# Kernel tuning notes

Hardware: AMD Instinct MI355X
Metric: run time of the kernel (lower is better)

## Reference

```python
import jax, jax.numpy as jnp
import numpy as np

RNN = 64

def linear(x, W, b):
    return x @ W.T + b

def sample_logprob(key, logits):
    # Categorical(softmax(logits)): sample + log_prob of the sample
    s = jax.random.categorical(key, logits)
    lp = jnp.take_along_axis(jax.nn.log_softmax(logits, -1), s[:, None], 1)[:, 0]
    return s, lp

def lstm_encode(inst, embed, W_ih, W_hh, b_ih, b_hh):
    # torch.nn.LSTMCell unrolled over the sequence; gate order i,f,g,o
    x = embed[inst]                              # [B,S,64]
    B = inst.shape[0]
    def step(carry, xt):
        h, c = carry
        gates = xt @ W_ih.T + b_ih + h @ W_hh.T + b_hh   # [B,256]
        i, f, g, o = jnp.split(gates, 4, axis=-1)
        c = jax.nn.sigmoid(f) * c + jax.nn.sigmoid(i) * jnp.tanh(g)
        h = jax.nn.sigmoid(o) * jnp.tanh(c)
        return (h, c), None
    h0 = jnp.zeros((B, RNN), x.dtype)
    (h, _), _ = jax.lax.scan(step, (h0, h0), jnp.swapaxes(x, 0, 1))
    return h

def setup_inputs():
    key = jax.random.key(0)
    ks = jax.random.split(key, 20)
    B, S, V = 16384, 32, 1000
    def nrm(k, shape, scale=0.05):
        return jax.random.normal(k, shape, jnp.float32) * scale
    return {
        "inst0": jax.random.randint(ks[0], (B, S), 0, V + 1),
        "inst1": jax.random.randint(ks[1], (B, S), 0, V + 1),
        "canvas0": jax.random.randint(ks[2], (B, 25, 4), 0, 5).astype(jnp.int32),
        "canvas1": jax.random.randint(ks[3], (B, 25, 4), 0, 5).astype(jnp.int32),
        "ref": jax.random.randint(ks[4], (B, 4), 0, 5).astype(jnp.int32),
        "embed": nrm(ks[5], (V + 1, RNN)),
        "W_ih": nrm(ks[6], (4 * RNN, RNN)), "W_hh": nrm(ks[7], (4 * RNN, RNN)),
        "b_ih": jnp.zeros(4 * RNN), "b_hh": jnp.zeros(4 * RNN),
        "Wc": nrm(ks[8], (3, RNN)), "bc": jnp.zeros(3),
        "Ws": nrm(ks[9], (3, RNN)), "bs": jnp.zeros(3),
        "Wl": nrm(ks[10], (25, RNN)), "bl": jnp.zeros(25),
        "Wr1": nrm(ks[11], (32, RNN + 4)), "br1": jnp.zeros(32),
        "Wr2": nrm(ks[12], (1, 32)), "br2": jnp.zeros(1),
        "Wp": nrm(ks[13], (8, RNN)), "bp": jnp.zeros(8),
    }

def reference(inst0, inst1, canvas0, canvas1, ref, embed, W_ih, W_hh, b_ih, b_hh,
              Wc, bc, Ws, bs, Wl, bl, Wr1, br1, Wr2, br2, Wp, bp):
    B = inst0.shape[0]
    kk = jax.random.split(jax.random.key(42), 7)
    final_canvas = canvas1                                   # [B,25,4]

    def step_rewards(loc_predict, color_sample, shape_sample):
        valid = (loc_predict >= 0) & (loc_predict < 25)
        pt = jnp.take_along_axis(final_canvas,
                                 jnp.clip(loc_predict, 0, 24)[:, None, None],
                                 axis=1)[:, 0]               # [B,4]
        ok = valid & (pt.sum(-1) >= 0)
        loc_r = jnp.where(ok, 1.0, -1.0)
        col_r = jnp.where(ok, jnp.where(color_sample == pt[:, 0], 1.0, -1.0), 0.0)
        shp_r = jnp.where(ok, jnp.where(shape_sample == pt[:, 1], 1.0, -1.0), 0.0)
        return loc_r, col_r, shp_r

    # ---- dialog step 0: absolute location ----
    h0 = lstm_encode(inst0, embed, W_ih, W_hh, b_ih, b_hh)
    cs0, clp0 = sample_logprob(kk[0], linear(h0, Wc, bc))
    ss0, slp0 = sample_logprob(kk[1], linear(h0, Ws, bs))
    loc0, llp0 = sample_logprob(kk[2], linear(h0, Wl, bl))
    loc_r0, col_r0, _ = step_rewards(loc0, cs0, ss0)

    # ---- dialog step 1: relative location w.r.t. attended ref object ----
    h1 = lstm_encode(inst1, embed, W_ih, W_hh, b_ih, b_hh)
    cs1, clp1 = sample_logprob(kk[3], linear(h1, Wc, bc))
    ss1, slp1 = sample_logprob(kk[4], linear(h1, Ws, bs))
    ls1, llp1 = sample_logprob(kk[5], linear(h1, Wp, bp))    # 8-way offset
    prev = canvas0.astype(h1.dtype)                          # [B,25,4]
    feat = jnp.concatenate([jnp.broadcast_to(h1[:, None, :], (B, 25, RNN)), prev], 2)  # [B,25,68]
    att_logits = (jax.nn.relu(feat @ Wr1.T + br1) @ Wr2.T + br2)[:, :, 0]              # [B,25]
    att_sample, alp1 = sample_logprob(kk[6], att_logits)
    ref_obj = jnp.take_along_axis(canvas0, att_sample[:, None, None], axis=1)[:, 0]    # [B,4]
    att_reward = ((ref_obj == ref).sum(-1) == 4).astype(jnp.float32) * 2.0 - 1.0
    offsets = jnp.array([[-1, 0], [1, 0], [0, 1], [0, -1],
                         [-1, -1], [-1, 1], [1, -1], [1, 1]], jnp.int32)
    off = offsets[ls1]
    loc1 = (ref_obj[:, 2] + off[:, 0]) * 5 + (ref_obj[:, 3] + off[:, 1])
    loc_r1, col_r1, _ = step_rewards(loc1, cs1, ss1)

    logp = jnp.stack([clp0, slp0, llp0, clp1, slp1, llp1, alp1])          # [7,B]
    # NB: original appends step_loc_reward into shape_rewards (kept verbatim)
    rew = jnp.stack([loc_r0, col_r0, loc_r0, loc_r1, col_r1, loc_r1, att_reward])  # [7,B]
    return logp, rew
```

## Files before the change

kernel.cpp:

```cpp
#include <hip/hip_runtime.h>
#include <hip/hip_bf16.h>
#include <stdint.h>
#include <math.h>

#define NB 16384
#define NSEQ 32
#define NV 1001
#define NROWS 32768

typedef __attribute__((ext_vector_type(8))) short bf16x8;
typedef __attribute__((ext_vector_type(4))) float f32x4;

__device__ __forceinline__ void tf2x32(uint32_t k0, uint32_t k1,
                                       uint32_t x0, uint32_t x1,
                                       uint32_t& o0, uint32_t& o1) {
  const uint32_t ks0 = k0, ks1 = k1, ks2 = k0 ^ k1 ^ 0x1BD11BDAu;
  x0 += ks0; x1 += ks1;
  const int rA[4] = {13, 15, 26, 6};
  const int rB[4] = {17, 29, 16, 24};
#pragma unroll
  for (int i = 0; i < 4; ++i) { x0 += x1; x1 = (x1 << rA[i]) | (x1 >> (32 - rA[i])); x1 ^= x0; }
  x0 += ks1; x1 += ks2 + 1u;
#pragma unroll
  for (int i = 0; i < 4; ++i) { x0 += x1; x1 = (x1 << rB[i]) | (x1 >> (32 - rB[i])); x1 ^= x0; }
  x0 += ks2; x1 += ks0 + 2u;
#pragma unroll
  for (int i = 0; i < 4; ++i) { x0 += x1; x1 = (x1 << rA[i]) | (x1 >> (32 - rA[i])); x1 ^= x0; }
  x0 += ks0; x1 += ks1 + 3u;
#pragma unroll
  for (int i = 0; i < 4; ++i) { x0 += x1; x1 = (x1 << rB[i]) | (x1 >> (32 - rB[i])); x1 ^= x0; }
  x0 += ks1; x1 += ks2 + 4u;
#pragma unroll
  for (int i = 0; i < 4; ++i) { x0 += x1; x1 = (x1 << rA[i]) | (x1 >> (32 - rA[i])); x1 ^= x0; }
  o0 = x0 + ks2; o1 = x1 + ks0 + 5u;
}

__device__ __forceinline__ float gumbel_from_bits(uint32_t bits) {
  uint32_t fb = (bits >> 9) | 0x3f800000u;
  float u = __uint_as_float(fb) - 1.0f;
  u = fmaxf(u, 1.17549435e-38f);
  return -logf(-logf(u));
}

__device__ __forceinline__ float sigm(float x) { return 1.0f / (1.0f + __expf(-x)); }
__device__ __forceinline__ float tanh_(float x) {
  float e = __expf(2.0f * x);
  return 1.0f - 2.0f / (e + 1.0f);
}

__device__ __forceinline__ float dot64(const float* __restrict__ w, const float* h) {
  float a = 0.f;
#pragma unroll
  for (int k = 0; k < 64; ++k) a = fmaf(w[k], h[k], a);
  return a;
}

__device__ __forceinline__ unsigned short bfbits(float x, float& xf) {
  __hip_bfloat16 hb = __float2bfloat16(x);
  xf = __bfloat162float(hb);
  unsigned short u;
  __builtin_memcpy(&u, &hb, 2);
  return u;
}

template <int N>
__device__ __forceinline__ void samp_team(const float* lg, int g, int C,
                                          uint32_t k0, uint32_t k1, int b,
                                          int& sOut, float& lpOut) {
  float m = -__builtin_inff();
#pragma unroll
  for (int i = 0; i < N; ++i) m = fmaxf(m, lg[i]);
  m = fmaxf(m, __shfl_xor(m, 1));
  m = fmaxf(m, __shfl_xor(m, 2));
  float se = 0.f;
#pragma unroll
  for (int i = 0; i < N; ++i) se += expf(lg[i] - m);
  se += __shfl_xor(se, 1);
  se += __shfl_xor(se, 2);
  const float lse = logf(se);
  float bz = -__builtin_inff(), bl = 0.f;
  int bi = 0x7fffffff;
#pragma unroll
  for (int i = 0; i < N; ++i) {
    const int c = g + 4 * i;
    uint32_t o0, o1; tf2x32(k0, k1, 0u, (uint32_t)(b * C + c), o0, o1);
    const float z = lg[i] + gumbel_from_bits(o0 ^ o1);
    if (z > bz || (z == bz && c < bi)) { bz = z; bi = c; bl = lg[i]; }
  }
#pragma unroll
  for (int d = 1; d <= 2; d <<= 1) {
    const float z2 = __shfl_xor(bz, d);
    const int i2 = __shfl_xor(bi, d);
    const float l2 = __shfl_xor(bl, d);
    if (z2 > bz || (z2 == bz && i2 < bi)) { bz = z2; bi = i2; bl = l2; }
  }
  sOut = bi;
  lpOut = (bl - m) - lse;
}

__global__ __launch_bounds__(256) void k_prep(
    const float* __restrict__ embed, const float* __restrict__ W_ih,
    const float* __restrict__ W_hh, const float* __restrict__ b_ih,
    const float* __restrict__ b_hh, float* __restrict__ embedWi,
    unsigned short* __restrict__ Wsp) {
  if (blockIdx.x >= NV) {
    int idx = (blockIdx.x - NV) * 256 + threadIdx.x;
    int s = idx >> 14;
    int rem = idx & 16383;
    int jp = rem >> 6, k = rem & 63;
    int j = (jp & 3) * 64 + (jp >> 2);
    float w = W_hh[j * 64 + k];
    float f1, f2, f3;
    unsigned short b1 = bfbits(w, f1);
    unsigned short b2 = bfbits(w - f1, f2);
    unsigned short b3 = bfbits(w - f1 - f2, f3);
    Wsp[idx] = (s == 0) ? b1 : (s == 1) ? b2 : b3;
    return;
  }
  __shared__ float er[64];
  int v = blockIdx.x;
  if (threadIdx.x < 64) er[threadIdx.x] = embed[v * 64 + threadIdx.x];
  __syncthreads();
  int jp = threadIdx.x;
  int j = (jp & 3) * 64 + (jp >> 2);
  float a = b_ih[j] + b_hh[j];
#pragma unroll
  for (int k = 0; k < 64; ++k) a = fmaf(W_ih[j * 64 + k], er[k], a);
  embedWi[v * 256 + jp] = a;
}

__global__ __launch_bounds__(512, 2) void k_lstm(
    const int* __restrict__ inst0, const int* __restrict__ inst1,
    const float* __restrict__ embedWi, const unsigned short* __restrict__ Wsp,
    float* __restrict__ hT) {
  extern __shared__ char smc[];
  int* idsb = (int*)(smc + 98304);

  const int tid = threadIdx.x;
  const int lane = tid & 63;
  const int wave = tid >> 6;
  const int wgj = wave >> 1;
  const int wrh = wave & 1;
  const int n15 = lane & 15;
  const int quad = lane >> 4;
  const int blk = blockIdx.x;
  const int rowbase = blk * 128;
  const int rb = rowbase & (NB - 1);
  const int* __restrict__ inst = (blk < 128) ? inst0 : inst1;

  bf16x8 afr[4][2][3];
#pragma unroll
  for (int jt = 0; jt < 4; ++jt) {
    const int jrow = (wgj * 4 + jt) * 16 + n15;
#pragma unroll
    for (int kc = 0; kc < 2; ++kc)
#pragma unroll
      for (int s = 0; s < 3; ++s)
        afr[jt][kc][s] =
            *(const bf16x8*)(Wsp + ((s * 256 + jrow) * 64 + kc * 32 + quad * 8));
  }

  for (int i = tid; i < 12288; i += 512) ((float*)smc)[i] = 0.f;
  if (tid < 128) idsb[tid] = inst[(rb + tid) * NSEQ];

  float cst[16];
#pragma unroll
  for (int i = 0; i < 16; ++i) cst[i] = 0.f;

  __syncthreads();

#pragma unroll 1
  for (int t = 0; t < NSEQ; ++t) {
    const char* __restrict__ hbr = smc + (t & 1) * 49152;
    char* __restrict__ hbw = smc + (((t & 1) ^ 1)) * 49152;

    int vv[4];
#pragma unroll
    for (int rt = 0; rt < 4; ++rt)
      vv[rt] = idsb[(t & 1) * 128 + wrh * 64 + rt * 16 + n15];
    if (tid < 128 && t + 1 < NSEQ)
      idsb[((t + 1) & 1) * 128 + tid] = inst[(rb + tid) * NSEQ + t + 1];

    f32x4 C[4][4];
#pragma unroll
    for (int jt = 0; jt < 4; ++jt)
#pragma unroll
      for (int rt = 0; rt < 4; ++rt) C[jt][rt] = (f32x4){0.f, 0.f, 0.f, 0.f};

#pragma unroll
    for (int rt = 0; rt < 4; ++rt) {
      const int rtg = wrh * 4 + rt;
      bf16x8 bfr[2][3];
#pragma unroll
      for (int kc = 0; kc < 2; ++kc)
#pragma unroll
        for (int s = 0; s < 3; ++s)
          bfr[kc][s] = *(const bf16x8*)(hbr + s * 16384 + rtg * 2048 +
                                        (kc * 4 + quad) * 256 + n15 * 16);
#pragma unroll
      for (int jt = 0; jt < 4; ++jt) {
#pragma unroll
        for (int kc = 0; kc < 2; ++kc) {
          f32x4 acc = C[jt][rt];
          acc = __builtin_amdgcn_mfma_f32_16x16x32_bf16(afr[jt][kc][1], bfr[kc][2], acc, 0, 0, 0);
          acc = __builtin_amdgcn_mfma_f32_16x16x32_bf16(afr[jt][kc][2], bfr[kc][1], acc, 0, 0, 0);
          acc = __builtin_amdgcn_mfma_f32_16x16x32_bf16(afr[jt][kc][0], bfr[kc][2], acc, 0, 0, 0);
          acc = __builtin_amdgcn_mfma_f32_16x16x32_bf16(afr[jt][kc][2], bfr[kc][0], acc, 0, 0, 0);
          acc = __builtin_amdgcn_mfma_f32_16x16x32_bf16(afr[jt][kc][1], bfr[kc][1], acc, 0, 0, 0);
          acc = __builtin_amdgcn_mfma_f32_16x16x32_bf16(afr[jt][kc][0], bfr[kc][1], acc, 0, 0, 0);
          acc = __builtin_amdgcn_mfma_f32_16x16x32_bf16(afr[jt][kc][1], bfr[kc][0], acc, 0, 0, 0);
          acc = __builtin_amdgcn_mfma_f32_16x16x32_bf16(afr[jt][kc][0], bfr[kc][0], acc, 0, 0, 0);
          C[jt][rt] = acc;
        }
      }
    }

    const bool last = (t == NSEQ - 1);
    float4 esA[4], esB[4];
#pragma unroll
    for (int rt = 0; rt < 4; ++rt)
      esA[rt] = *(const float4*)(embedWi + vv[rt] * 256 + (wgj * 16 + 0 * 4 + quad) * 4);
#pragma unroll
    for (int jt = 0; jt < 4; ++jt) {
      if (jt < 3) {
#pragma unroll
        for (int rt = 0; rt < 4; ++rt)
          esB[rt] = *(const float4*)(embedWi + vv[rt] * 256 +
                                     (wgj * 16 + (jt + 1) * 4 + quad) * 4);
      }
      const int u = wgj * 16 + jt * 4 + quad;
#pragma unroll
      for (int rt = 0; rt < 4; ++rt) {
        const int r = wrh * 64 + rt * 16 + n15;
        const float gi = C[jt][rt].x + esA[rt].x;
        const float gf = C[jt][rt].y + esA[rt].y;
        const float gg = C[jt][rt].z + esA[rt].z;
        const float go = C[jt][rt].w + esA[rt].w;
        const float ci = sigm(gf) * cst[jt * 4 + rt] + sigm(gi) * tanh_(gg);
        cst[jt * 4 + rt] = ci;
        const float h = sigm(go) * tanh_(ci);
        float f1, f2, f3;
        const unsigned short b1 = bfbits(h, f1);
        const unsigned short b2 = bfbits(h - f1, f2);
        const unsigned short b3 = bfbits(h - f1 - f2, f3);
        const int coff = (r >> 4) * 2048 + (u >> 3) * 256 + (r & 15) * 16 + (u & 7) * 2;
        *(unsigned short*)(hbw + 0 * 16384 + coff) = b1;
        *(unsigned short*)(hbw + 1 * 16384 + coff) = b2;
        *(unsigned short*)(hbw + 2 * 16384 + coff) = b3;
        if (last) hT[u * NROWS + rowbase + r] = h;
      }
#pragma unroll
      for (int rt = 0; rt < 4; ++rt) esA[rt] = esB[rt];
    }
    __syncthreads();
  }
}

__global__ __launch_bounds__(256) void k_heads(
    const int* __restrict__ canvas0, const int* __restrict__ canvas1,
    const int* __restrict__ ref,
    const float* __restrict__ Wc, const float* __restrict__ bc,
    const float* __restrict__ Ws, const float* __restrict__ bs,
    const float* __restrict__ Wl, const float* __restrict__ bl,
    const float* __restrict__ Wr1, const float* __restrict__ br1,
    const float* __restrict__ Wr2, const float* __restrict__ br2,
    const float* __restrict__ Wp, const float* __restrict__ bp,
    const float* __restrict__ hT, float* __restrict__ out) {
  const int tid = threadIdx.x;
  const int g = tid & 3;
  const int s = blockIdx.x & 1;
  const int b = (blockIdx.x >> 1) * 64 + (tid >> 2);
  const float NEG = -__builtin_inff();

  uint32_t kk0[7], kk1[7];
#pragma unroll
  for (int i = 0; i < 7; ++i) {
    uint32_t o0, o1; tf2x32(0u, 42u, 0u, (uint32_t)i, o0, o1);
    kk0[i] = o0; kk1[i] = o1;
  }

  float h[64];
#pragma unroll
  for (int u = 0; u < 64; ++u) h[u] = hT[u * NROWS + s * NB + b];

  float lgc[1], lgs[1];
  lgc[0] = (g < 3) ? (bc[g] + dot64(Wc + g * 64, h)) : NEG;
  lgs[0] = (g < 3) ? (bs[g] + dot64(Ws + g * 64, h)) : NEG;

  if (s == 0) {
    int cs0, ss0, loc0; float clp0, slp0, llp0;
    samp_team<1>(lgc, g, 3, kk0[0], kk1[0], b, cs0, clp0);
    samp_team<1>(lgs, g, 3, kk0[1], kk1[1], b, ss0, slp0);
    float lgl[7];
#pragma unroll
    for (int i = 0; i < 7; ++i) {
      const int cc = g + 4 * i;
      lgl[i] = (cc < 25) ? (bl[cc] + dot64(Wl + cc * 64, h)) : NEG;
    }
    samp_team<7>(lgl, g, 25, kk0[2], kk1[2], b, loc0, llp0);

    if (g == 0) {
      const int p0 = min(max(loc0, 0), 24);
      const int4 pt = ((const int4*)(canvas1 + b * 100))[p0];
      const bool ok0 = (loc0 >= 0) && (loc0 < 25) && (pt.x + pt.y + pt.z + pt.w >= 0);
      const float loc_r0 = ok0 ? 1.f : -1.f;
      const float col_r0 = ok0 ? ((cs0 == pt.x) ? 1.f : -1.f) : 0.f;
      out[0 * NB + b] = clp0;
      out[1 * NB + b] = slp0;
      out[2 * NB + b] = llp0;
      out[7 * NB + b] = loc_r0;
      out[8 * NB + b] = col_r0;
      out[9 * NB + b] = loc_r0;
    }
  } else {
    int cs1, ss1, ls1; float clp1, slp1, llp1;
    samp_team<1>(lgc, g, 3, kk0[3], kk1[3], b, cs1, clp1);
    samp_team<1>(lgs, g, 3, kk0[4], kk1[4], b, ss1, slp1);
    float lgp[2];
#pragma unroll
    for (int i = 0; i < 2; ++i) {
      const int cc = g + 4 * i;
      lgp[i] = bp[cc] + dot64(Wp + cc * 64, h);
    }
    samp_team<2>(lgp, g, 8, kk0[5], kk1[5], b, ls1, llp1);

    float uv8[8], w64[8], w65[8], w66[8], w67[8], wr2[8];
#pragma unroll
    for (int i = 0; i < 8; ++i) {
      const int j = g + 4 * i;
      uv8[i] = br1[j] + dot64(Wr1 + j * 68, h);
      const float* wr = Wr1 + j * 68 + 64;
      w64[i] = wr[0]; w65[i] = wr[1]; w66[i] = wr[2]; w67[i] = wr[3];
      wr2[i] = Wr2[j];
    }
    float lgA[7];
#pragma unroll
    for (int i = 0; i < 7; ++i) lgA[i] = NEG;
    const float b2 = br2[0];
#pragma unroll
    for (int p = 0; p < 25; ++p) {
      const int4 c4 = ((const int4*)(canvas0 + b * 100))[p];
      const float f0 = (float)c4.x, f1 = (float)c4.y;
      const float f2 = (float)c4.z, f3 = (float)c4.w;
      float part = 0.f;
#pragma unroll
      for (int i = 0; i < 8; ++i) {
        float hj = uv8[i];
        hj = fmaf(w64[i], f0, hj);
        hj = fmaf(w65[i], f1, hj);
        hj = fmaf(w66[i], f2, hj);
        hj = fmaf(w67[i], f3, hj);
        part = fmaf(wr2[i], fmaxf(hj, 0.f), part);
      }
      part += __shfl_xor(part, 1);
      part += __shfl_xor(part, 2);
      const float ap = b2 + part;
      if ((p & 3) == g) lgA[p >> 2] = ap;
    }
    int att_s; float alp1;
    samp_team<7>(lgA, g, 25, kk0[6], kk1[6], b, att_s, alp1);

    if (g == 0) {
      const int4 r4 = ((const int4*)(canvas0 + b * 100))[att_s];
      const int4 rr = *(const int4*)(ref + b * 4);
      const bool match = (r4.x == rr.x) && (r4.y == rr.y) &&
                         (r4.z == rr.z) && (r4.w == rr.w);
      const float att_reward = match ? 1.f : -1.f;
      const int ox = (int)((0x22001120u >> (ls1 * 4)) & 0xFu) - 1;
      const int oy = (int)((0x20200211u >> (ls1 * 4)) & 0xFu) - 1;
      const int loc1 = (r4.z + ox) * 5 + (r4.w + oy);
      const int p1 = min(max(loc1, 0), 24);
      const int4 q4 = ((const int4*)(canvas1 + b * 100))[p1];
      const bool ok1 = (loc1 >= 0) && (loc1 < 25) && (q4.x + q4.y + q4.z + q4.w >= 0);
      const float loc_r1 = ok1 ? 1.f : -1.f;
      const float col_r1 = ok1 ? ((cs1 == q4.x) ? 1.f : -1.f) : 0.f;
      out[3 * NB + b]  = clp1;
      out[4 * NB + b]  = slp1;
      out[5 * NB + b]  = llp1;
      out[6 * NB + b]  = alp1;
      out[10 * NB + b] = loc_r1;
      out[11 * NB + b] = col_r1;
      out[12 * NB + b] = loc_r1;
      out[13 * NB + b] = att_reward;
    }
  }
}

extern "C" void kernel_launch(void* const* d_in, const int* in_sizes, int n_in,
                              void* d_out, int out_size, void* d_ws, size_t ws_size,
                              hipStream_t stream) {
  const int* inst0 = (const int*)d_in[0];
  const int* inst1 = (const int*)d_in[1];
  const int* canvas0 = (const int*)d_in[2];
  const int* canvas1 = (const int*)d_in[3];
  const int* ref = (const int*)d_in[4];
  const float* embed = (const float*)d_in[5];
  const float* W_ih = (const float*)d_in[6];
  const float* W_hh = (const float*)d_in[7];
  const float* b_ih = (const float*)d_in[8];
  const float* b_hh = (const float*)d_in[9];
  const float* Wc = (const float*)d_in[10];
  const float* bc = (const float*)d_in[11];
  const float* Ws = (const float*)d_in[12];
  const float* bs = (const float*)d_in[13];
  const float* Wl = (const float*)d_in[14];
  const float* bl = (const float*)d_in[15];
  const float* Wr1 = (const float*)d_in[16];
  const float* br1 = (const float*)d_in[17];
  const float* Wr2 = (const float*)d_in[18];
  const float* br2 = (const float*)d_in[19];
  const float* Wp = (const float*)d_in[20];
  const float* bp = (const float*)d_in[21];

  float* ws = (float*)d_ws;
  float* embedWi = ws;
  unsigned short* Wsp = (unsigned short*)(ws + NV * 256);
  float* hT = ws + NV * 256 + 24576;
  float* out = (float*)d_out;

  (void)hipFuncSetAttribute((const void*)k_lstm,
                            hipFuncAttributeMaxDynamicSharedMemorySize, 163840);

  k_prep<<<NV + 192, 256, 0, stream>>>(embed, W_ih, W_hh, b_ih, b_hh, embedWi, Wsp);
  k_lstm<<<256, 512, 99328, stream>>>(inst0, inst1, embedWi, Wsp, hT);
  k_heads<<<512, 256, 0, stream>>>(canvas0, canvas1, ref, Wc, bc, Ws, bs,
                                   Wl, bl, Wr1, br1, Wr2, br2, Wp, bp, hT, out);
}
```

Measured before the change: 472.5 us.

## Pad LSTM hidden-state LDS layout and pack h stores as 32-bit words

The LDS layout of the bf16-split hidden state is padded (272-byte chunks instead of 256) to reduce bank conflicts. W_hh columns are permuted in prep so each lane can write two adjacent hidden units as one 32-bit store instead of separate 16-bit stores. The epilogue loop order is swapped so all four jt values for a row tile are gathered together, and an asm barrier pins the A fragments in registers. LDS use grows slightly, and the k permutation must stay consistent between the weight and h layouts.

```diff
diff --git a/kernel.cpp b/kernel.cpp
--- a/kernel.cpp
+++ b/kernel.cpp
@@ -7,6 +7,11 @@
 #define NSEQ 32
 #define NV 1001
 #define NROWS 32768
+
+#define CHK 272
+#define RTG (8 * CHK)
+#define SPL (8 * RTG)
+#define HBUF (3 * SPL)
 
 typedef __attribute__((ext_vector_type(8))) short bf16x8;
 typedef __attribute__((ext_vector_type(4))) float f32x4;
@@ -107,7 +112,9 @@
     int idx = (blockIdx.x - NV) * 256 + threadIdx.x;
     int s = idx >> 14;
     int rem = idx & 16383;
-    int jp = rem >> 6, k = rem & 63;
+    int jp = rem >> 6, m = rem & 63;
+    int kc = m >> 5, q = (m >> 3) & 3, p = m & 7;
+    int k = kc * 32 + q * 8 + ((p >> 1) + ((p & 1) << 2));
     int j = (jp & 3) * 64 + (jp >> 2);
     float w = W_hh[j * 64 + k];
     float f1, f2, f3;
@@ -134,7 +141,7 @@
     const float* __restrict__ embedWi, const unsigned short* __restrict__ Wsp,
     float* __restrict__ hT) {
   extern __shared__ char smc[];
-  int* idsb = (int*)(smc + 98304);
+  int* idsb = (int*)(smc + 2 * HBUF);
 
   const int tid = threadIdx.x;
   const int lane = tid & 63;
@@ -159,8 +166,15 @@
         afr[jt][kc][s] =
             *(const bf16x8*)(Wsp + ((s * 256 + jrow) * 64 + kc * 32 + quad * 8));
   }
-
-  for (int i = tid; i < 12288; i += 512) ((float*)smc)[i] = 0.f;
+#pragma unroll
+  for (int jt = 0; jt < 4; ++jt)
+#pragma unroll
+    for (int kc = 0; kc < 2; ++kc)
+#pragma unroll
+      for (int s = 0; s < 3; ++s)
+        asm volatile("" : "+v"(afr[jt][kc][s]));
+
+  for (int i = tid; i < HBUF / 4; i += 512) ((float*)smc)[i] = 0.f;
   if (tid < 128) idsb[tid] = inst[(rb + tid) * NSEQ];
 
   float cst[16];
@@ -171,8 +185,8 @@
 
 #pragma unroll 1
   for (int t = 0; t < NSEQ; ++t) {
-    const char* __restrict__ hbr = smc + (t & 1) * 49152;
-    char* __restrict__ hbw = smc + (((t & 1) ^ 1)) * 49152;
+    const char* __restrict__ hbr = smc + (t & 1) * HBUF;
+    char* __restrict__ hbw = smc + ((t & 1) ^ 1) * HBUF;
 
     int vv[4];
 #pragma unroll
@@ -195,8 +209,8 @@
       for (int kc = 0; kc < 2; ++kc)
 #pragma unroll
         for (int s = 0; s < 3; ++s)
-          bfr[kc][s] = *(const bf16x8*)(hbr + s * 16384 + rtg * 2048 +
-                                        (kc * 4 + quad) * 256 + n15 * 16);
+          bfr[kc][s] = *(const bf16x8*)(hbr + s * SPL + rtg * RTG +
+                                        (kc * 4 + quad) * CHK + n15 * 16);
 #pragma unroll
       for (int jt = 0; jt < 4; ++jt) {
 #pragma unroll
@@ -218,39 +232,49 @@
     const bool last = (t == NSEQ - 1);
     float4 esA[4], esB[4];
 #pragma unroll
-    for (int rt = 0; rt < 4; ++rt)
-      esA[rt] = *(const float4*)(embedWi + vv[rt] * 256 + (wgj * 16 + 0 * 4 + quad) * 4);
-#pragma unroll
-    for (int jt = 0; jt < 4; ++jt) {
-      if (jt < 3) {
-#pragma unroll
-        for (int rt = 0; rt < 4; ++rt)
-          esB[rt] = *(const float4*)(embedWi + vv[rt] * 256 +
-                                     (wgj * 16 + (jt + 1) * 4 + quad) * 4);
+    for (int jt = 0; jt < 4; ++jt)
+      esA[jt] = *(const float4*)(embedWi + vv[0] * 256 + (wgj * 16 + jt * 4 + quad) * 4);
+#pragma unroll
+    for (int rt = 0; rt < 4; ++rt) {
+      if (rt < 3) {
+#pragma unroll
+        for (int jt = 0; jt < 4; ++jt)
+          esB[jt] = *(const float4*)(embedWi + vv[rt + 1] * 256 +
+                                     (wgj * 16 + jt * 4 + quad) * 4);
       }
-      const int u = wgj * 16 + jt * 4 + quad;
-#pragma unroll
-      for (int rt = 0; rt < 4; ++rt) {
-        const int r = wrh * 64 + rt * 16 + n15;
-        const float gi = C[jt][rt].x + esA[rt].x;
-        const float gf = C[jt][rt].y + esA[rt].y;
-        const float gg = C[jt][rt].z + esA[rt].z;
-        const float go = C[jt][rt].w + esA[rt].w;
+      const int r = wrh * 64 + rt * 16 + n15;
+      const int rtg = wrh * 4 + rt;
+      float hval[4];
+      unsigned short s1[4], s2[4], s3[4];
+#pragma unroll
+      for (int jt = 0; jt < 4; ++jt) {
+        const float gi = C[jt][rt].x + esA[jt].x;
+        const float gf = C[jt][rt].y + esA[jt].y;
+        const float gg = C[jt][rt].z + esA[jt].z;
+        const float go = C[jt][rt].w + esA[jt].w;
         const float ci = sigm(gf) * cst[jt * 4 + rt] + sigm(gi) * tanh_(gg);
         cst[jt * 4 + rt] = ci;
         const float h = sigm(go) * tanh_(ci);
+        hval[jt] = h;
         float f1, f2, f3;
-        const unsigned short b1 = bfbits(h, f1);
-        const unsigned short b2 = bfbits(h - f1, f2);
-        const unsigned short b3 = bfbits(h - f1 - f2, f3);
-        const int coff = (r >> 4) * 2048 + (u >> 3) * 256 + (r & 15) * 16 + (u & 7) * 2;
-        *(unsigned short*)(hbw + 0 * 16384 + coff) = b1;
-        *(unsigned short*)(hbw + 1 * 16384 + coff) = b2;
-        *(unsigned short*)(hbw + 2 * 16384 + coff) = b3;
-        if (last) hT[u * NROWS + rowbase + r] = h;
+        s1[jt] = bfbits(h, f1);
+        s2[jt] = bfbits(h - f1, f2);
+        s3[jt] = bfbits(h - f1 - f2, f3);
       }
-#pragma unroll
-      for (int rt = 0; rt < 4; ++rt) esA[rt] = esB[rt];
+      char* base = hbw + rtg * RTG + n15 * 16 + quad * 4;
+      *(uint32_t*)(base + 0 * SPL + (wgj * 2 + 0) * CHK) = (uint32_t)s1[0] | ((uint32_t)s1[1] << 16);
+      *(uint32_t*)(base + 0 * SPL + (wgj * 2 + 1) * CHK) = (uint32_t)s1[2] | ((uint32_t)s1[3] << 16);
+      *(uint32_t*)(base + 1 * SPL + (wgj * 2 + 0) * CHK) = (uint32_t)s2[0] | ((uint32_t)s2[1] << 16);
+      *(uint32_t*)(base + 1 * SPL + (wgj * 2 + 1) * CHK) = (uint32_t)s2[2] | ((uint32_t)s2[3] << 16);
+      *(uint32_t*)(base + 2 * SPL + (wgj * 2 + 0) * CHK) = (uint32_t)s3[0] | ((uint32_t)s3[1] << 16);
+      *(uint32_t*)(base + 2 * SPL + (wgj * 2 + 1) * CHK) = (uint32_t)s3[2] | ((uint32_t)s3[3] << 16);
+      if (last) {
+#pragma unroll
+        for (int jt = 0; jt < 4; ++jt)
+          hT[(wgj * 16 + jt * 4 + quad) * NROWS + rowbase + r] = hval[jt];
+      }
+#pragma unroll
+      for (int jt = 0; jt < 4; ++jt) esA[jt] = esB[jt];
     }
     __syncthreads();
   }
@@ -421,8 +445,9 @@
   (void)hipFuncSetAttribute((const void*)k_lstm,
                             hipFuncAttributeMaxDynamicSharedMemorySize, 163840);
 
+  const size_t ldsBytes = 2 * HBUF + 1024;
   k_prep<<<NV + 192, 256, 0, stream>>>(embed, W_ih, W_hh, b_ih, b_hh, embedWi, Wsp);
-  k_lstm<<<256, 512, 99328, stream>>>(inst0, inst1, embedWi, Wsp, hT);
+  k_lstm<<<256, 512, ldsBytes, stream>>>(inst0, inst1, embedWi, Wsp, hT);
   k_heads<<<512, 256, 0, stream>>>(canvas0, canvas1, ref, Wc, bc, Ws, bs,
                                    Wl, bl, Wr1, br1, Wr2, br2, Wp, bp, hT, out);
 }
```

Measured after the change: 482.9 us. 2.2% more time.
